# Optimization experiments

Hardware: AMD Instinct MI355X
Metric: run time of the kernel (lower is better)

Reference implementation:

```python
import jax, jax.numpy as jnp
import numpy as np

B, S, HIDDEN = 2, 4096, 4096
NUM_HEADS = 32
QK_NOPE = 128
QK_ROPE = 64
QK_HEAD = QK_NOPE + QK_ROPE
KV_LORA = 512
Q_LORA = 1536


def setup_inputs() -> dict:
    key = jax.random.key(0)
    k1, k2, k3, k4, k5, k6 = jax.random.split(key, 6)
    x = jax.random.normal(k1, (B, S, HIDDEN), dtype=jnp.float32)
    cos = jax.random.uniform(k2, (B, S, QK_ROPE), dtype=jnp.float32)
    sin = jax.random.uniform(k3, (B, S, QK_ROPE), dtype=jnp.float32)
    # Linear weights, torch layout [out, in]
    Wqa = jax.random.normal(k4, (Q_LORA, HIDDEN), dtype=jnp.float32) * 0.02
    Wqb = jax.random.normal(k5, (NUM_HEADS * QK_HEAD, Q_LORA), dtype=jnp.float32) * 0.02
    Wkva = jax.random.normal(k6, (KV_LORA + QK_ROPE, HIDDEN), dtype=jnp.float32) * 0.02
    return {"x": x, "cos": cos, "sin": sin, "Wqa": Wqa, "Wqb": Wqb, "Wkva": Wkva}


def _rotate_half(t):
    d = t.shape[-1] // 2
    return jnp.concatenate([-t[..., d:], t[..., :d]], axis=-1)


def reference(x, cos, sin, Wqa, Wqb, Wkva):
    b, s, _ = x.shape
    # low-rank Q: x -> q_lora -> heads*(nope+rope)
    q = jnp.einsum('bsh,rh->bsr', x, Wqa)
    q = jnp.einsum('bsr,or->bso', q, Wqb).reshape(b, s, NUM_HEADS, QK_HEAD)
    q_nope = q[..., :QK_NOPE]
    q_pe = q[..., QK_NOPE:]
    # KV down-projection with MQA rope part
    kv = jnp.einsum('bsh,oh->bso', x, Wkva)
    compressed_kv = kv[..., :KV_LORA]                         # [b,s,kv_lora]
    k_pe = kv[..., KV_LORA:].reshape(b, s, 1, QK_ROPE)
    # NeoX explicit RoPE, unsqueeze_dim=2
    c = cos[:, :, None, :]
    sn = sin[:, :, None, :]
    q_pe_rot = q_pe * c + _rotate_half(q_pe) * sn
    k_pe_rot = k_pe * c + _rotate_half(k_pe) * sn
    q_out = jnp.concatenate([q_nope, q_pe_rot], axis=-1).reshape(b, s, -1)
    k_out = k_pe_rot.reshape(b, s, QK_ROPE)
    return jnp.concatenate([q_out, k_out, compressed_kv], axis=-1)
```

## Files before the change

### kernel.cpp

```cpp
#include <hip/hip_runtime.h>
#include <hip/hip_bf16.h>
#include <stdint.h>

typedef __bf16 bf16x8 __attribute__((ext_vector_type(8)));
typedef float f32x4 __attribute__((ext_vector_type(4)));
typedef float fvec4 __attribute__((ext_vector_type(4)));
typedef unsigned short usvec4 __attribute__((ext_vector_type(4)));
typedef unsigned int ui32x4 __attribute__((ext_vector_type(4)));

#define AS3 __attribute__((address_space(3)))
#define AS1 __attribute__((address_space(1)))

static __device__ __forceinline__ unsigned short f2bf(float f) {
  unsigned int u = __float_as_uint(f);
  u += 0x7FFF + ((u >> 16) & 1);
  return (unsigned short)(u >> 16);
}


extern "C" __global__ void cvt_bf16_kernel(const float* __restrict__ src,
                                           unsigned short* __restrict__ dst,
                                           long n4) {
  long i = (long)blockIdx.x * blockDim.x + threadIdx.x;
  const long stride = (long)gridDim.x * blockDim.x;
  for (; i < n4; i += stride) {
    const fvec4 v = __builtin_nontemporal_load(&((const fvec4*)src)[i]);
    usvec4 o;
    o.x = f2bf(v.x); o.y = f2bf(v.y); o.z = f2bf(v.z); o.w = f2bf(v.w);
    ((usvec4*)dst)[i] = o;
  }
}

extern "C" __global__ void cvt_pad_kernel(const float* __restrict__ src,
                                          unsigned short* __restrict__ dst,
                                          long nsrc4, long ntot4) {
  long i = (long)blockIdx.x * blockDim.x + threadIdx.x;
  const long stride = (long)gridDim.x * blockDim.x;
  for (; i < ntot4; i += stride) {
    usvec4 o = {0, 0, 0, 0};
    if (i < nsrc4) {
      const fvec4 v = __builtin_nontemporal_load(&((const fvec4*)src)[i]);
      o.x = f2bf(v.x); o.y = f2bf(v.y); o.z = f2bf(v.z); o.w = f2bf(v.w);
    }
    ((usvec4*)dst)[i] = o;
  }
}


template <int MODE>
__global__ __launch_bounds__(512, 2)
void mla_gemm(const __hip_bfloat16* __restrict__ A0p,
              const __hip_bfloat16* __restrict__ B0p, int K0,
              const __hip_bfloat16* __restrict__ A1p,
              const __hip_bfloat16* __restrict__ B1p,
              unsigned short* __restrict__ qlora,
              const float* __restrict__ cosp,
              const float* __restrict__ sinp,
              float* __restrict__ out) {
  extern __shared__ __align__(128) char lds[];
  const int tid = threadIdx.x;
  const int lane = tid & 63;
  const int w = tid >> 6;
  const int wm = w >> 2, wn = w & 3;
  const int l15 = lane & 15, lhi = lane >> 4;
  const int srow8 = lane >> 3;
  const int swzc = ((lane & 7) ^ srow8) * 8;

  const __hip_bfloat16* Aptr;
  const __hip_bfloat16* Bptr;
  int K, bm, bn;
  bool isA2 = false;
  if constexpr (MODE == 0) {
    const int swz = ((int)blockIdx.x & 7) * 32 + ((int)blockIdx.x >> 3);
    bm = swz >> 3; bn = swz & 7;
    Aptr = A0p; Bptr = B0p; K = K0;
  } else {
    const int bid = (int)blockIdx.x;
    if (bid < 32) {
      isA2 = true; bm = bid; bn = 8; Aptr = A1p; Bptr = B1p; K = 4096;
    } else {
      const int b2 = bid - 32;
      const int swz = (b2 & 7) * 96 + (b2 >> 3);
      bm = swz / 24; bn = swz - bm * 24;
      Aptr = A0p; Bptr = B0p; K = K0;
    }
  }
  const long brow = (long)bm * 256;
  const int bcol = bn * 256;

  const __hip_bfloat16* aSt = Aptr + (brow + w * 16 + srow8) * (long)K + swzc;
  const __hip_bfloat16* bSt = Bptr + ((long)bcol + srow8) * (long)K + swzc;
  const int wj0 = w * 16, wj1 = w * 16 + 8;
  const int cb_j0 = (2 * (wj0 >> 5)) * 32 + (wj0 & 31);
  const int cb_j1 = (2 * (wj1 >> 5)) * 32 + (wj1 & 31);
  const int ldsWj = w * 2048;

  const int aRdRow = (wm * 64 + l15) * 128;
  const int bRdRow = (wn * 32 + l15) * 128;
  const int ck0 = (lhi ^ (l15 & 7)) * 16;

  f32x4 acc[8][4] = {};
  bf16x8 aF[4][2];
  bf16x8 bF[2][2][2];

  const int T = K >> 6;
  const int I = T >> 1;

  auto stage = [&](int u, int kt) {
    const int b = kt & 1;
    if (u < 2) {
      const int off = b * 32768 + u * 16384 + ldsWj;
      __builtin_amdgcn_global_load_lds((AS1 void*)(aSt + (long)(u * 128) * K + kt * 64),
                                       (AS3 void*)(lds + off), 16, 0, 0);
      __builtin_amdgcn_global_load_lds((AS1 void*)(aSt + (long)(u * 128 + 8) * K + kt * 64),
                                       (AS3 void*)(lds + off + 1024), 16, 0, 0);
    } else {
      const int h = u - 2;
      const int off = 65536 + b * 32768 + h * 16384 + ldsWj;
      __builtin_amdgcn_global_load_lds((AS1 void*)(bSt + (long)(cb_j0 + h * 32) * K + kt * 64),
                                       (AS3 void*)(lds + off), 16, 0, 0);
      __builtin_amdgcn_global_load_lds((AS1 void*)(bSt + (long)(cb_j1 + h * 32) * K + kt * 64),
                                       (AS3 void*)(lds + off + 1024), 16, 0, 0);
    }
  };
  auto readA = [&](int qh, int b) {
    const int base = b * 32768 + qh * 16384 + aRdRow;
    #pragma unroll
    for (int fr = 0; fr < 4; ++fr) {
      aF[fr][0] = *(const bf16x8*)(lds + base + fr * 2048 + ck0);
      aF[fr][1] = *(const bf16x8*)(lds + base + fr * 2048 + (ck0 ^ 64));
    }
  };
  auto readB = [&](int c, int b) {
    const int base = 65536 + b * 32768 + c * 16384 + bRdRow;
    #pragma unroll
    for (int fq = 0; fq < 2; ++fq) {
      bF[c][fq][0] = *(const bf16x8*)(lds + base + fq * 2048 + ck0);
      bF[c][fq][1] = *(const bf16x8*)(lds + base + fq * 2048 + (ck0 ^ 64));
    }
  };
  auto mmac = [&](int qh, int c) {
    __builtin_amdgcn_s_setprio(1);
    #pragma unroll
    for (int fr = 0; fr < 4; ++fr)
      #pragma unroll
      for (int fq = 0; fq < 2; ++fq) {
        acc[qh * 4 + fr][c * 2 + fq] = __builtin_amdgcn_mfma_f32_16x16x32_bf16(
            aF[fr][0], bF[c][fq][0], acc[qh * 4 + fr][c * 2 + fq], 0, 0, 0);
        acc[qh * 4 + fr][c * 2 + fq] = __builtin_amdgcn_mfma_f32_16x16x32_bf16(
            aF[fr][1], bF[c][fq][1], acc[qh * 4 + fr][c * 2 + fq], 0, 0, 0);
      }
    __builtin_amdgcn_s_setprio(0);
  };
  #define BAR() __builtin_amdgcn_s_barrier()
  #define LGKM0() do { asm volatile("s_waitcnt lgkmcnt(0)" ::: "memory"); \
                       __builtin_amdgcn_sched_barrier(0); } while (0)

  stage(0, 0); stage(1, 0); stage(2, 0); stage(3, 0);
  stage(0, 1); stage(3, 1);
  asm volatile("s_waitcnt vmcnt(4)" ::: "memory");
  BAR();

  for (int i = 0; i < I; ++i) {
    const int ktB = 2 * i + 1;
    const bool more = (i < I - 1);
    readA(0, 0); readB(0, 0); stage(1, ktB);
    BAR(); LGKM0(); mmac(0, 0); BAR();
    readB(1, 0); stage(2, ktB);
    BAR(); LGKM0(); mmac(0, 1); BAR();
    readA(1, 0); if (more) stage(0, ktB + 1);
    BAR(); LGKM0(); mmac(1, 1); BAR();
    if (more) stage(3, ktB + 1);
    BAR(); LGKM0(); mmac(1, 0);
    if (more) asm volatile("s_waitcnt vmcnt(4)" ::: "memory");
    else      asm volatile("s_waitcnt vmcnt(0)" ::: "memory");
    BAR();
    readA(0, 1); readB(0, 1); if (more) stage(1, ktB + 1);
    BAR(); LGKM0(); mmac(0, 0); BAR();
    readB(1, 1); if (more) stage(2, ktB + 1);
    BAR(); LGKM0(); mmac(0, 1); BAR();
    readA(1, 1); if (more) stage(0, ktB + 2);
    BAR(); LGKM0(); mmac(1, 1); BAR();
    if (more) stage(3, ktB + 2);
    BAR(); LGKM0(); mmac(1, 0);
    if (more) asm volatile("s_waitcnt vmcnt(4)" ::: "memory");
    else      asm volatile("s_waitcnt vmcnt(0)" ::: "memory");
    BAR();
  }

  const int wcol = bcol + wn * 64;
  const long rbase = brow + wm * 64;
  char* eplds = lds + w * 4096;

  auto storeTileF32 = [&](int i8, float* dst, bool rope) {
    #pragma unroll
    for (int j = 0; j < 4; ++j)
      #pragma unroll
      for (int r = 0; r < 4; ++r) {
        float v = acc[i8][j][r];
        if (rope) {
          const long row = rbase + (i8 >> 2) * 128 + (i8 & 3) * 16 + lhi * 4 + r;
          const int d = (j >> 1) * 32 + (j & 1) * 16 + l15;
          const float rot = (j < 2) ? -acc[i8][j + 2][r] : acc[i8][j - 2][r];
          v = v * cosp[row * 64 + d] + rot * sinp[row * 64 + d];
        }
        *(float*)(eplds + (lhi * 4 + r) * 256 + ((j >> 1) * 32 + (j & 1) * 16 + l15) * 4) = v;
      }
    asm volatile("s_waitcnt lgkmcnt(0)" ::: "memory");
    #pragma unroll
    for (int t = 0; t < 4; ++t) {
      const int r16 = t * 4 + (lane >> 4);
      const f32x4 v = *(const f32x4*)(eplds + r16 * 256 + (lane & 15) * 16);
      const long row = rbase + (i8 >> 2) * 128 + (i8 & 3) * 16 + r16;
      __builtin_nontemporal_store(v, (f32x4*)(dst + row * 6720 + (lane & 15) * 4));
    }
  };
  auto storeTileBf16 = [&](int i8) {
    #pragma unroll
    for (int j = 0; j < 4; ++j)
      #pragma unroll
      for (int r = 0; r < 4; ++r)
        *(unsigned short*)(eplds + (lhi * 4 + r) * 128 +
                           ((j >> 1) * 32 + (j & 1) * 16 + l15) * 2) = f2bf(acc[i8][j][r]);
    asm volatile("s_waitcnt lgkmcnt(0)" ::: "memory");
    #pragma unroll
    for (int t = 0; t < 2; ++t) {
      const int r16 = t * 8 + (lane >> 3);
      const ui32x4 v = *(const ui32x4*)(eplds + r16 * 128 + (lane & 7) * 16);
      const long row = rbase + (i8 >> 2) * 128 + (i8 & 3) * 16 + r16;
      *(ui32x4*)((char*)qlora + (row * 1536 + wcol) * 2 + (lane & 7) * 16) = v;
    }
  };

  if constexpr (MODE == 0) {
    if (wcol < 1536) {
      #pragma unroll
      for (int i8 = 0; i8 < 8; ++i8) storeTileBf16(i8);
    } else {
      #pragma unroll
      for (int i8 = 0; i8 < 8; ++i8) storeTileF32(i8, out + wcol + 4672, false);
    }
  } else {
    if (isA2) {
      if (wn == 0) {
        #pragma unroll
        for (int i8 = 0; i8 < 8; ++i8) storeTileF32(i8, out + 6144, true);
      }
    } else if ((wcol % 192) != 128) {
      #pragma unroll
      for (int i8 = 0; i8 < 8; ++i8) storeTileF32(i8, out + wcol, false);
    } else {
      #pragma unroll
      for (int i8 = 0; i8 < 8; ++i8) storeTileF32(i8, out + wcol, true);
    }
  }
  #undef BAR
  #undef LGKM0
}


extern "C" void kernel_launch(void* const* d_in, const int* in_sizes, int n_in,
                              void* d_out, int out_size, void* d_ws, size_t ws_size,
                              hipStream_t stream) {
  const float* x    = (const float*)d_in[0];
  const float* cosp = (const float*)d_in[1];
  const float* sinp = (const float*)d_in[2];
  const float* Wqa  = (const float*)d_in[3];
  const float* Wqb  = (const float*)d_in[4];
  const float* Wkva = (const float*)d_in[5];
  float* out = (float*)d_out;

  char* ws = (char*)d_ws;
  __hip_bfloat16* xb  = (__hip_bfloat16*)ws;
  __hip_bfloat16* w1  = (__hip_bfloat16*)(ws + 67108864L);
  __hip_bfloat16* wqb = (__hip_bfloat16*)(ws + 67108864L + 17825792L);
  unsigned short* ql  = (unsigned short*)(ws + 67108864L + 17825792L + 18874368L);

  cvt_bf16_kernel<<<2048, 256, 0, stream>>>(x,   (unsigned short*)xb,  8192L * 4096 / 4);
  cvt_bf16_kernel<<<1024, 256, 0, stream>>>(Wqa, (unsigned short*)w1,  1536L * 4096 / 4);
  cvt_pad_kernel<<<640, 256, 0, stream>>>(Wkva, (unsigned short*)(w1 + 1536L * 4096),
                                          576L * 4096 / 4, 640L * 4096 / 4);
  cvt_bf16_kernel<<<1024, 256, 0, stream>>>(Wqb, (unsigned short*)wqb, 6144L * 1536 / 4);

  (void)hipFuncSetAttribute((const void*)&mla_gemm<0>,
                            hipFuncAttributeMaxDynamicSharedMemorySize, 131072);
  (void)hipFuncSetAttribute((const void*)&mla_gemm<1>,
                            hipFuncAttributeMaxDynamicSharedMemorySize, 131072);

  mla_gemm<0><<<dim3(256), 512, 131072, stream>>>(xb, w1, 4096, nullptr, nullptr,
                                                  ql, cosp, sinp, out);
  mla_gemm<1><<<dim3(800), 512, 131072, stream>>>((const __hip_bfloat16*)ql, wqb, 1536,
                                                  xb, w1, ql, cosp, sinp, out);
}
```

Measured before the change: 362.6 us.

## Deepen GEMM prefetch pipeline to two full k-tiles ahead with finer vmcnt waits

```diff
diff --git a/kernel.cpp b/kernel.cpp
--- a/kernel.cpp
+++ b/kernel.cpp
@@ -46,6 +46,11 @@
   }
 }
 
+
+#define VMW(N) asm volatile("s_waitcnt vmcnt(" #N ")" ::: "memory")
+#define BAR() __builtin_amdgcn_s_barrier()
+#define LGKM0() do { asm volatile("s_waitcnt lgkmcnt(0)" ::: "memory"); \
+                     __builtin_amdgcn_sched_barrier(0); } while (0)
 
 template <int MODE>
 __global__ __launch_bounds__(512, 2)
@@ -152,41 +157,45 @@
       }
     __builtin_amdgcn_s_setprio(0);
   };
-  #define BAR() __builtin_amdgcn_s_barrier()
-  #define LGKM0() do { asm volatile("s_waitcnt lgkmcnt(0)" ::: "memory"); \
-                       __builtin_amdgcn_sched_barrier(0); } while (0)
-
-  stage(0, 0); stage(1, 0); stage(2, 0); stage(3, 0);
-  stage(0, 1); stage(3, 1);
-  asm volatile("s_waitcnt vmcnt(4)" ::: "memory");
+
+  stage(0, 0); stage(2, 0); stage(3, 0); stage(1, 0);
+  stage(0, 1); stage(2, 1); stage(3, 1); stage(1, 1);
+  VMW(12);
   BAR();
 
-  for (int i = 0; i < I; ++i) {
-    const int ktB = 2 * i + 1;
-    const bool more = (i < I - 1);
-    readA(0, 0); readB(0, 0); stage(1, ktB);
-    BAR(); LGKM0(); mmac(0, 0); BAR();
-    readB(1, 0); stage(2, ktB);
-    BAR(); LGKM0(); mmac(0, 1); BAR();
-    readA(1, 0); if (more) stage(0, ktB + 1);
+  for (int i = 0; i < I - 1; ++i) {
+    const int e2 = 2 * i + 2, o2 = 2 * i + 3;
+    readA(0, 0); readB(0, 0);
+    BAR(); LGKM0(); mmac(0, 0); VMW(10); BAR();
+    readB(1, 0); stage(0, e2); stage(2, e2);
+    BAR(); LGKM0(); mmac(0, 1); VMW(12); BAR();
+    readA(1, 0); stage(3, e2);
     BAR(); LGKM0(); mmac(1, 1); BAR();
-    if (more) stage(3, ktB + 1);
-    BAR(); LGKM0(); mmac(1, 0);
-    if (more) asm volatile("s_waitcnt vmcnt(4)" ::: "memory");
-    else      asm volatile("s_waitcnt vmcnt(0)" ::: "memory");
-    BAR();
-    readA(0, 1); readB(0, 1); if (more) stage(1, ktB + 1);
-    BAR(); LGKM0(); mmac(0, 0); BAR();
-    readB(1, 1); if (more) stage(2, ktB + 1);
-    BAR(); LGKM0(); mmac(0, 1); BAR();
-    readA(1, 1); if (more) stage(0, ktB + 2);
+    stage(1, e2);
+    BAR(); LGKM0(); mmac(1, 0); VMW(12); BAR();
+    readA(0, 1); readB(0, 1);
+    BAR(); LGKM0(); mmac(0, 0); VMW(10); BAR();
+    readB(1, 1); stage(0, o2); stage(2, o2);
+    BAR(); LGKM0(); mmac(0, 1); VMW(12); BAR();
+    readA(1, 1); stage(3, o2);
     BAR(); LGKM0(); mmac(1, 1); BAR();
-    if (more) stage(3, ktB + 2);
-    BAR(); LGKM0(); mmac(1, 0);
-    if (more) asm volatile("s_waitcnt vmcnt(4)" ::: "memory");
-    else      asm volatile("s_waitcnt vmcnt(0)" ::: "memory");
-    BAR();
-  }
+    stage(1, o2);
+    BAR(); LGKM0(); mmac(1, 0); VMW(12); BAR();
+  }
+  readA(0, 0); readB(0, 0);
+  BAR(); LGKM0(); mmac(0, 0); VMW(10); BAR();
+  readB(1, 0);
+  BAR(); LGKM0(); mmac(0, 1); VMW(8); BAR();
+  readA(1, 0);
+  BAR(); LGKM0(); mmac(1, 1); BAR();
+  BAR(); LGKM0(); mmac(1, 0); VMW(4); BAR();
+  readA(0, 1); readB(0, 1);
+  BAR(); LGKM0(); mmac(0, 0); VMW(2); BAR();
+  readB(1, 1);
+  BAR(); LGKM0(); mmac(0, 1); VMW(0); BAR();
+  readA(1, 1);
+  BAR(); LGKM0(); mmac(1, 1); BAR();
+  BAR(); LGKM0(); mmac(1, 0); BAR();
 
   const int wcol = bcol + wn * 64;
   const long rbase = brow + wm * 64;
@@ -254,8 +263,6 @@
       for (int i8 = 0; i8 < 8; ++i8) storeTileF32(i8, out + wcol, true);
     }
   }
-  #undef BAR
-  #undef LGKM0
 }
 
 
```

Result: no change. 358.4 us (-1.1%).
